# Kernel optimization log

Hardware: AMD Instinct MI355X
Metric: run time of the kernel (lower is better)

The kernel has to match this reference:

```python
import jax, jax.numpy as jnp
import numpy as np

INIT_L = 512.0
EPS = 1e-6
N_HEAD = 16


def fire_bias(T, w1, b1, w2, b2, c, L_multiplier):
    # positions and relative distances
    pos = jnp.arange(T, dtype=jnp.float32)
    rel = pos[:, None] - pos[None, :]                      # (T, T)
    threshold = jnp.abs(L_multiplier * INIT_L)
    pos_norm = jnp.maximum(pos, threshold)[:, None]        # (T, 1)
    rel = jnp.log(jnp.abs(c * rel) + 1.0)                  # (T, T)
    pos_norm = jnp.log(jnp.abs(c * pos_norm) + 1.0) + EPS  # (T, 1)
    nd = rel / pos_norm                                    # (T, T)
    # tiny MLP: 1 -> mlp_width -> n_head
    h = jax.nn.relu(nd[..., None] * w1[0] + b1)            # (T, T, 32)
    bias = jnp.einsum('tsw,wh->hts', h, w2) + b2[:, None, None]  # (H, T, T)
    causal = jnp.tril(jnp.ones((T, T), dtype=bool))
    bias = jnp.where(causal[None], bias, -jnp.inf)
    return bias[None]                                      # (1, H, T, T)


def reference(x, Wqkv, bqkv, Wproj, bproj, w1, b1, w2, b2, c_param, L_multiplier):
    B, T, C = x.shape
    H = N_HEAD
    hd = C // H
    qkv = x @ Wqkv + bqkv                                  # (B, T, 3C)
    q, k, v = jnp.split(qkv, 3, axis=-1)
    q = q.reshape(B, T, H, hd).transpose(0, 2, 1, 3)       # (B, H, T, hd)
    k = k.reshape(B, T, H, hd).transpose(0, 2, 1, 3)
    v = v.reshape(B, T, H, hd).transpose(0, 2, 1, 3)
    bias = fire_bias(T, w1, b1, w2, b2, c_param, L_multiplier)  # (1, H, T, T)
    scale = 1.0 / jnp.sqrt(jnp.float32(hd))
    att = jnp.einsum('bhqd,bhkd->bhqk', q, k) * scale + bias
    att = jax.nn.softmax(att, axis=-1)
    y = jnp.einsum('bhqk,bhkd->bhqd', att, v)              # (B, H, T, hd)
    y = y.transpose(0, 2, 1, 3).reshape(B, T, C)
    return y @ Wproj + bproj


def setup_inputs() -> dict:
    key = jax.random.key(0)
    ks = jax.random.split(key, 8)
    B, T, C, H, W = 2, 2048, 1024, 16, 32
    s = 0.02
    return {
        'x': jax.random.normal(ks[0], (B, T, C), jnp.float32),
        'Wqkv': jax.random.normal(ks[1], (C, 3 * C), jnp.float32) * s,
        'bqkv': jnp.zeros((3 * C,), jnp.float32),
        'Wproj': jax.random.normal(ks[2], (C, C), jnp.float32) * s,
        'bproj': jnp.zeros((C,), jnp.float32),
        'w1': jax.random.normal(ks[3], (1, W), jnp.float32),
        'b1': jnp.zeros((W,), jnp.float32),
        'w2': jax.random.normal(ks[4], (W, H), jnp.float32) * 0.1,
        'b2': jnp.zeros((H,), jnp.float32),
        'c_param': jnp.float32(0.1),
        'L_multiplier': jnp.float32(1.0),
    }
```

## Files before the change

kernel.cpp:

```cpp
#include <hip/hip_runtime.h>
#include <cstdint>

typedef unsigned short u16;
typedef unsigned int u32;

typedef short bf16x8 __attribute__((ext_vector_type(8)));
typedef float f32x4 __attribute__((ext_vector_type(4)));

#define LN2 0.69314718055994530942f
#define LOG2E 1.44269504088896340736f
#define INFF __builtin_inff()

__device__ __forceinline__ u16 f2bf(float f) {
  u32 u = __float_as_uint(f);
  u = (u + 0x7fffu + ((u >> 16) & 1u)) >> 16;
  return (u16)u;
}
__device__ __forceinline__ u32 pack2bf(float a, float b) {
  u32 ta = __float_as_uint(a) + 0x8000u;
  u32 tb = __float_as_uint(b) + 0x8000u;
  return __builtin_amdgcn_perm(tb, ta, 0x07060302u);
}
__device__ __forceinline__ u32 pack2bf_rne(float a, float b) {
  return (u32)f2bf(a) | ((u32)f2bf(b) << 16);
}

#if __has_builtin(__builtin_amdgcn_global_load_lds)
#define HAVE_GLDS 1
__device__ __forceinline__ void glds16(const u16* g, u16* l) {
  __builtin_amdgcn_global_load_lds((const __attribute__((address_space(1))) void*)g,
                                   (__attribute__((address_space(3))) void*)l, 16, 0, 0);
}
#else
#define HAVE_GLDS 0
#endif

__device__ __forceinline__ void stage1k(const u16* gperlane, u16* lwave, int lane) {
#if HAVE_GLDS
  (void)lane;
  glds16(gperlane, lwave);
#else
  *(uint4*)(lwave + lane * 8) = *(const uint4*)gperlane;
#endif
}

__device__ __forceinline__ u16* swzp(u16* base, int row, int bc) {
  return (u16*)((char*)base + row * 128 + (bc ^ ((row & 7) << 4)));
}


__global__ void k_convert_x(const float* __restrict__ in, u16* __restrict__ out, int n4) {
  int i = blockIdx.x * blockDim.x + threadIdx.x;
  if (i < n4) {
    float4 v = ((const float4*)in)[i];
    ushort4 o;
    o.x = f2bf(v.x); o.y = f2bf(v.y); o.z = f2bf(v.z); o.w = f2bf(v.w);
    ((ushort4*)out)[i] = o;
  }
}

__global__ void k_transpose_bf(const float* __restrict__ in, u16* __restrict__ out, int R, int C) {
  __shared__ float t[32][33];
  int c0 = blockIdx.x * 32, r0 = blockIdx.y * 32;
  int tx = threadIdx.x, ty = threadIdx.y;
#pragma unroll
  for (int k = 0; k < 4; k++) t[ty + 8 * k][tx] = in[(size_t)(r0 + ty + 8 * k) * C + c0 + tx];
  __syncthreads();
#pragma unroll
  for (int k = 0; k < 4; k++) out[(size_t)(c0 + ty + 8 * k) * R + r0 + tx] = f2bf(t[tx][ty + 8 * k]);
}

__global__ void k_tables(const float* __restrict__ cP, const float* __restrict__ lP,
                         float* __restrict__ ig2, float* __restrict__ rl) {
  int t = blockIdx.x * blockDim.x + threadIdx.x;
  float c = fabsf(cP[0]);
  if (t < 2048) {
    float lm = lP[0];
    float thr = fabsf(lm * 512.0f);
    float pn = fmaxf((float)t, thr);
    float den = logf(c * pn + 1.0f) + 1e-6f;
    ig2[t] = LN2 / den;
  }
  if (t < 2112) {
    int d = t - 63;
    if (d < 0) d = 0;
    rl[t] = log2f(c * (float)d + 1.0f);
  }
}

__global__ void k_segments(const float* __restrict__ w1, const float* __restrict__ b1,
                           const float* __restrict__ w2, const float* __restrict__ b2,
                           float* __restrict__ segX, float* __restrict__ segA,
                           float* __restrict__ segB, int* __restrict__ segU) {
  __shared__ float xs[32];
  __shared__ float srt[32];
  __shared__ float uniq[32];
  __shared__ int uCnt;
  int t = threadIdx.x;
  if (t < 32) {
    float w = w1[t], b = b1[t];
    xs[t] = (w != 0.0f) ? (-b / w) : INFF;
  }
  __syncthreads();
  if (t < 32) {
    float x = xs[t];
    int r = 0;
    for (int v = 0; v < 32; v++) {
      float xv = xs[v];
      if (xv < x || (xv == x && v < t)) r++;
    }
    srt[r] = x;
  }
  __syncthreads();
  if (t == 0) {
    int u = 0;
    for (int i = 0; i < 32; i++) {
      float v = srt[i];
      if (v < 3.0e38f && (u == 0 || v != uniq[u - 1])) uniq[u++] = v;
    }
    uCnt = u;
    segU[0] = u;
  }
  __syncthreads();
  int u = uCnt;
  if (t < u) segX[t] = uniq[t];
  for (int idx = t; idx < (u + 1) * 16; idx += blockDim.x) {
    int j = idx >> 4, h = idx & 15;
    float p;
    if (u == 0) p = 0.0f;
    else if (j == 0) p = uniq[0] - 1.0f;
    else if (j == u) p = uniq[u - 1] + 1.0f;
    else p = 0.5f * (uniq[j - 1] + uniq[j]);
    float A = b2[h], B = 0.0f;
    for (int w = 0; w < 32; w++) {
      float w1w = w1[w], b1w = b1[w], w2wh = w2[w * 16 + h];
      if (w1w != 0.0f) {
        if (fmaf(w1w, p, b1w) > 0.0f) { B += w1w * w2wh; A += b1w * w2wh; }
      } else if (b1w > 0.0f) {
        A += b1w * w2wh;
      }
    }
    segA[j * 16 + h] = A;
    segB[j * 16 + h] = B;
  }
}

template <int MODE, int BN>
__launch_bounds__(256, 3)
__global__ void k_gemm(const u16* __restrict__ A, const u16* __restrict__ BT,
                       const float* __restrict__ bias, float* __restrict__ outF,
                       u16* __restrict__ outQ, u16* __restrict__ outK, u16* __restrict__ outV,
                       int M, int N, int K) {
  constexpr int NT = BN / 32;
  constexpr int NCH = BN / 32;
  __shared__ u16 As[128 * 64];
  __shared__ u16 Bs[BN * 64];
  const int tid = threadIdx.x;
  const int lane = tid & 63, wave = tid >> 6;
  const int li = lane & 15, quad = lane >> 4;
  const int wrow = (wave >> 1) * 64, wcol = (wave & 1) * (BN / 2);
  const int rb = blockIdx.y * 128, cb = blockIdx.x * BN;

  f32x4 acc[4][NT];
#pragma unroll
  for (int i = 0; i < 4; i++)
#pragma unroll
    for (int j = 0; j < NT; j++) acc[i][j] = (f32x4){0.f, 0.f, 0.f, 0.f};

#if HAVE_GLDS
  const u16* gA = A + (size_t)(rb + (tid >> 3)) * K + (tid & 7) * 8;
  const u16* gB = BT + (size_t)(cb + (tid >> 3)) * K + (tid & 7) * 8;
  u16* lA = As + wave * 512;
  u16* lB = Bs + wave * 512;

  for (int k0 = 0; k0 < K; k0 += 64) {
    __syncthreads();
#pragma unroll
    for (int ch = 0; ch < 4; ch++) glds16(gA + (size_t)ch * 32 * K + k0, lA + ch * 2048);
#pragma unroll
    for (int ch = 0; ch < NCH; ch++) glds16(gB + (size_t)ch * 32 * K + k0, lB + ch * 2048);
    __syncthreads();
#pragma unroll
    for (int c = 0; c < 2; c++) {
      bf16x8 af[4], bfr[NT];
#pragma unroll
      for (int mt = 0; mt < 4; mt++)
        af[mt] = *(const bf16x8*)(&As[(wrow + mt * 16 + li) * 64 + c * 32 + quad * 8]);
#pragma unroll
      for (int nt = 0; nt < NT; nt++)
        bfr[nt] = *(const bf16x8*)(&Bs[(wcol + nt * 16 + li) * 64 + c * 32 + quad * 8]);
#pragma unroll
      for (int mt = 0; mt < 4; mt++)
#pragma unroll
        for (int nt = 0; nt < NT; nt++)
          acc[mt][nt] = __builtin_amdgcn_mfma_f32_16x16x32_bf16(af[mt], bfr[nt], acc[mt][nt], 0, 0, 0);
    }
  }
#else
  for (int k0 = 0; k0 < K; k0 += 64) {
    __syncthreads();
    for (int idx = tid * 8; idx < 128 * 64; idx += 256 * 8) {
      int rr = idx >> 6, cc = idx & 63;
      *(uint4*)(&As[idx]) = *(const uint4*)(A + (size_t)(rb + rr) * K + k0 + cc);
    }
    for (int idx = tid * 8; idx < BN * 64; idx += 256 * 8) {
      int rr = idx >> 6, cc = idx & 63;
      *(uint4*)(&Bs[idx]) = *(const uint4*)(BT + (size_t)(cb + rr) * K + k0 + cc);
    }
    __syncthreads();
#pragma unroll
    for (int c = 0; c < 2; c++) {
      bf16x8 af[4], bfr[NT];
#pragma unroll
      for (int mt = 0; mt < 4; mt++)
        af[mt] = *(const bf16x8*)(&As[(wrow + mt * 16 + li) * 64 + c * 32 + quad * 8]);
#pragma unroll
      for (int nt = 0; nt < NT; nt++)
        bfr[nt] = *(const bf16x8*)(&Bs[(wcol + nt * 16 + li) * 64 + c * 32 + quad * 8]);
#pragma unroll
      for (int mt = 0; mt < 4; mt++)
#pragma unroll
        for (int nt = 0; nt < NT; nt++)
          acc[mt][nt] = __builtin_amdgcn_mfma_f32_16x16x32_bf16(af[mt], bfr[nt], acc[mt][nt], 0, 0, 0);
    }
  }
#endif

#pragma unroll
  for (int mt = 0; mt < 4; mt++)
#pragma unroll
    for (int nt = 0; nt < NT; nt++) {
      const int col = cb + wcol + nt * 16 + li;
      const int row0 = rb + wrow + mt * 16 + quad * 4;
      float v[4];
#pragma unroll
      for (int r = 0; r < 4; r++) v[r] = acc[mt][nt][r] + bias[col];
      if (MODE == 0) {
        const int bb = row0 >> 11, tt0 = row0 & 2047;
        const int sel = col >> 10, w = col & 1023, hh = w >> 6, dd = w & 63;
        if (sel == 0) {
          u16* dst = outQ + ((size_t)((bb * 16 + hh) * 2048 + tt0)) * 64 + dd;
#pragma unroll
          for (int r = 0; r < 4; r++) dst[(size_t)r * 64] = f2bf(v[r]);
        } else if (sel == 1) {
          u16* base = outK + ((size_t)((bb * 16 + hh) * 2048 + tt0)) * 64;
#pragma unroll
          for (int r = 0; r < 4; r++) {
            int tt = tt0 + r;
            base[(size_t)r * 64 + (dd ^ (((tt & 7)) << 3))] = f2bf(v[r]);
          }
        } else {
          u16* vrow = outV + ((size_t)((bb * 16 + hh) * 64 + dd)) * 2048;
          uint2 pk;
          pk.x = pack2bf_rne(v[0], v[1]);
          pk.y = pack2bf_rne(v[2], v[3]);
          *(uint2*)(vrow + (tt0 ^ ((dd & 7) << 3))) = pk;
        }
      } else {
#pragma unroll
        for (int r = 0; r < 4; r++) outF[(size_t)(row0 + r) * N + col] = v[r];
      }
    }
}

__launch_bounds__(256, 3)
__global__ void k_attn(const u16* __restrict__ Q, const u16* __restrict__ K,
                       const u16* __restrict__ Vt, u16* __restrict__ Y,
                       const float* __restrict__ ig2, const float* __restrict__ RL,
                       const float* __restrict__ segX, const float* __restrict__ segA,
                       const float* __restrict__ segB, const int* __restrict__ segU) {
  __shared__ u16 KsB[2 * 64 * 64];
  __shared__ u16 VtsB[2 * 64 * 64];
  __shared__ u16 Ps[64 * 64];
  __shared__ float rls[2112];
  __shared__ float sXl[32];
  __shared__ float sAl[33];
  __shared__ float sBl[33];

  const int xi = blockIdx.x, h = blockIdx.y, b = blockIdx.z;
  const int q0b = xi >> 1;
  const int flip = (xi & 1) ^ ((h >> 3) & 1);
  const int qt = flip ? (31 - q0b) : q0b;

  const int tid = threadIdx.x, lane = tid & 63, wave = tid >> 6;
  const int li = lane & 15, quad = lane >> 4;
  const int bh = b * 16 + h;
  const u16* Qg = Q + (size_t)bh * 2048 * 64;
  const u16* Kg = K + (size_t)bh * 2048 * 64;
  const u16* Vg = Vt + (size_t)bh * 64 * 2048;

  for (int i = tid; i < 2112; i += 256) rls[i] = RL[i];

  const int u = segU[0];
  float x0 = INFF, A0, B0, A1, B1;
  A0 = segA[h]; B0 = segB[h]; A1 = A0; B1 = B0;
  if (u == 1) { x0 = segX[0]; A1 = segA[16 + h]; B1 = segB[16 + h]; }
  if (u > 1) {
    if (tid < u) sXl[tid] = segX[tid];
    if (tid < u + 1) { sAl[tid] = segA[tid * 16 + h]; sBl[tid] = segB[tid * 16 + h]; }
  }
  const float A0e = A0 * LOG2E, A1e = A1 * LOG2E;
  const float SCL = 0.125f * LOG2E;

  const int t = qt * 64 + wave * 16 + li;
  bf16x8 qf[2];
#pragma unroll
  for (int c = 0; c < 2; c++)
    qf[c] = *(const bf16x8*)(Qg + (size_t)t * 64 + c * 32 + quad * 8);

  const float gI = ig2[t];
  const float x0r = x0 / gI;
  const float B0g = B0 * gI * LOG2E, B1g = B1 * gI * LOG2E;
  const bool uniB = (u <= 1) && (x0r <= 0.0f) && (A0e == A1e);
  float mrow = -INFF, lrow = 0.0f;
  f32x4 oacc[4];
#pragma unroll
  for (int nt = 0; nt < 4; nt++) oacc[nt] = (f32x4){0.f, 0.f, 0.f, 0.f};

  const u16* kgB = Kg + (size_t)(wave * 16 + (lane >> 3)) * 64 + (lane & 7) * 8;
  const u16* vgB = Vg + (size_t)(wave * 16 + (lane >> 3)) * 2048 + (lane & 7) * 8;

  auto stage = [&](int buf, int kt2) {
    u16* kd = KsB + buf * 4096 + wave * 1024;
    const u16* kg = kgB + (size_t)kt2 * 4096;
    stage1k(kg, kd, lane);
    stage1k(kg + 8 * 64, kd + 512, lane);
    u16* vd = VtsB + buf * 4096 + wave * 1024;
    const u16* vg = vgB + kt2 * 64;
    stage1k(vg, vd, lane);
    stage1k(vg + 8 * 2048, vd + 512, lane);
  };

  stage(0, 0);
  int cur = 0;

  for (int kt = 0; kt <= qt; kt++) {
    const int kb = kt * 64;
    __syncthreads();
    if (kt < qt) stage(cur ^ 1, kt + 1);

    u16* KsT = KsB + cur * 4096;
    u16* VtT = VtsB + cur * 4096;

    f32x4 sacc[4];
#pragma unroll
    for (int nt = 0; nt < 4; nt++) sacc[nt] = (f32x4){0.f, 0.f, 0.f, 0.f};
#pragma unroll
    for (int c = 0; c < 2; c++)
#pragma unroll
      for (int nt = 0; nt < 4; nt++) {
        bf16x8 kf = *(const bf16x8*)swzp(KsT, nt * 16 + li, c * 64 + quad * 16);
        sacc[nt] = __builtin_amdgcn_mfma_f32_16x16x32_bf16(kf, qf[c], sacc[nt], 0, 0, 0);
      }

    const int Cbase = t - kb - quad * 4 + 63;
    const float* rp = &rls[Cbase - 51];
    const int lim = Cbase - 63;
    if (uniB) {
#pragma unroll
      for (int nt = 0; nt < 4; nt++)
#pragma unroll
        for (int r = 0; r < 4; r++) {
          float z = fmaf(rp[51 - nt * 16 - r], B1g, sacc[nt][r] * SCL);
          if (kt == qt) z = (nt * 16 + r > lim) ? -INFF : z;
          sacc[nt][r] = z;
        }
    } else if (u <= 1) {
#pragma unroll
      for (int nt = 0; nt < 4; nt++)
#pragma unroll
        for (int r = 0; r < 4; r++) {
          float rlv = rp[51 - nt * 16 - r];
          bool hi = rlv > x0r;
          float z = fmaf(rlv, hi ? B1g : B0g, hi ? A1e : A0e);
          z = fmaf(sacc[nt][r], SCL, z);
          if (kt == qt) z = (nt * 16 + r > lim) ? -INFF : z;
          sacc[nt][r] = z;
        }
    } else {
#pragma unroll
      for (int nt = 0; nt < 4; nt++)
#pragma unroll
        for (int r = 0; r < 4; r++) {
          float nd = rp[51 - nt * 16 - r] * gI;
          int j = 0;
          for (int i = 0; i < u; i++) j += (nd > sXl[i]) ? 1 : 0;
          float z = (fmaf(nd, sBl[j], sAl[j]) + sacc[nt][r] * 0.125f) * LOG2E;
          if (kt == qt) z = (nt * 16 + r > lim) ? -INFF : z;
          sacc[nt][r] = z;
        }
    }

    f32x4 mm = sacc[0];
#pragma unroll
    for (int nt = 1; nt < 4; nt++)
#pragma unroll
      for (int r = 0; r < 4; r++) mm[r] = fmaxf(mm[r], sacc[nt][r]);
    float vm = fmaxf(fmaxf(mm[0], mm[1]), fmaxf(mm[2], mm[3]));
    vm = fmaxf(vm, __shfl_xor(vm, 16, 64));
    vm = fmaxf(vm, __shfl_xor(vm, 32, 64));
    float mnew = fmaxf(mrow, vm);
    bool grew = mnew > mrow;
    float alpha = __builtin_amdgcn_exp2f(mrow - mnew);
    mrow = mnew;
#pragma unroll
    for (int nt = 0; nt < 4; nt++)
#pragma unroll
      for (int r = 0; r < 4; r++)
        sacc[nt][r] = __builtin_amdgcn_exp2f(sacc[nt][r] - mnew);
    f32x4 sv = (sacc[0] + sacc[1]) + (sacc[2] + sacc[3]);
    float s = (sv[0] + sv[1]) + (sv[2] + sv[3]);
    s += __shfl_xor(s, 16, 64);
    s += __shfl_xor(s, 32, 64);
    lrow = lrow * alpha + s;
    if (__any(grew)) {
#pragma unroll
      for (int nt = 0; nt < 4; nt++)
#pragma unroll
        for (int r = 0; r < 4; r++) oacc[nt][r] *= alpha;
    }

    const int prow = wave * 16 + li;
#pragma unroll
    for (int nt = 0; nt < 4; nt++) {
      uint2 pk;
      pk.x = pack2bf(sacc[nt][0], sacc[nt][1]);
      pk.y = pack2bf(sacc[nt][2], sacc[nt][3]);
      *(uint2*)swzp(Ps, prow, 32 * nt + 8 * quad) = pk;
    }

#pragma unroll
    for (int c = 0; c < 2; c++) {
      bf16x8 pf = *(const bf16x8*)swzp(Ps, prow, c * 64 + quad * 16);
#pragma unroll
      for (int nt = 0; nt < 4; nt++) {
        bf16x8 vf = *(const bf16x8*)swzp(VtT, nt * 16 + li, c * 64 + quad * 16);
        oacc[nt] = __builtin_amdgcn_mfma_f32_16x16x32_bf16(vf, pf, oacc[nt], 0, 0, 0);
      }
    }
    cur ^= 1;
  }

  float inv = 1.0f / lrow;
  u16* dst = Y + (size_t)(b * 2048 + t) * 1024 + h * 64 + quad * 4;
#pragma unroll
  for (int nt = 0; nt < 4; nt++) {
    uint2 pk;
    pk.x = pack2bf(oacc[nt][0] * inv, oacc[nt][1] * inv);
    pk.y = pack2bf(oacc[nt][2] * inv, oacc[nt][3] * inv);
    *(uint2*)(dst + nt * 16) = pk;
  }
}

extern "C" void kernel_launch(void* const* d_in, const int* in_sizes, int n_in,
                              void* d_out, int out_size, void* d_ws, size_t ws_size,
                              hipStream_t stream) {
  (void)in_sizes; (void)n_in; (void)out_size; (void)ws_size;
  const float* x = (const float*)d_in[0];
  const float* Wqkv = (const float*)d_in[1];
  const float* bqkv = (const float*)d_in[2];
  const float* Wproj = (const float*)d_in[3];
  const float* bproj = (const float*)d_in[4];
  const float* w1 = (const float*)d_in[5];
  const float* b1 = (const float*)d_in[6];
  const float* w2 = (const float*)d_in[7];
  const float* b2 = (const float*)d_in[8];
  const float* cP = (const float*)d_in[9];
  const float* lP = (const float*)d_in[10];

  char* ws = (char*)d_ws;
  u16* Xbf = (u16*)(ws);
  u16* WqkvT = (u16*)(ws + (size_t)(8 << 20));
  u16* WprojT = (u16*)(ws + (size_t)(14 << 20));
  u16* Qb = (u16*)(ws + (size_t)(16 << 20));
  u16* Kb = (u16*)(ws + (size_t)(24 << 20));
  u16* Vb = (u16*)(ws + (size_t)(32 << 20));
  u16* Yb = (u16*)(ws + (size_t)(40 << 20));
  float* IG = (float*)(ws + (size_t)(48 << 20));
  float* RL = IG + 2048;
  float* SEGX = RL + 2112;
  float* SEGA = SEGX + 32;
  float* SEGB = SEGA + 33 * 16;
  int* SEGU = (int*)(SEGB + 33 * 16);

  k_convert_x<<<4096, 256, 0, stream>>>(x, Xbf, 1048576);
  k_transpose_bf<<<dim3(96, 32), dim3(32, 8), 0, stream>>>(Wqkv, WqkvT, 1024, 3072);
  k_transpose_bf<<<dim3(32, 32), dim3(32, 8), 0, stream>>>(Wproj, WprojT, 1024, 1024);
  k_tables<<<9, 256, 0, stream>>>(cP, lP, IG, RL);
  k_segments<<<1, 64, 0, stream>>>(w1, b1, w2, b2, SEGX, SEGA, SEGB, SEGU);

  k_gemm<0, 128><<<dim3(24, 32), 256, 0, stream>>>(Xbf, WqkvT, bqkv, nullptr, Qb, Kb, Vb,
                                                   4096, 3072, 1024);
  k_attn<<<dim3(32, 16, 2), 256, 0, stream>>>(Qb, Kb, Vb, Yb, IG, RL, SEGX, SEGA, SEGB, SEGU);
  k_gemm<1, 64><<<dim3(16, 32), 256, 0, stream>>>(Yb, WprojT, bproj, (float*)d_out, nullptr,
                                                  nullptr, nullptr, 4096, 1024, 1024);
}
```

Measured before the change: 239.9 us.

## Process two query tiles per attention block and compute log distances inline

Result: slower. 247.3 us (+3.1%).

```diff
diff --git a/kernel.cpp b/kernel.cpp
--- a/kernel.cpp
+++ b/kernel.cpp
@@ -71,7 +71,7 @@
 }
 
 __global__ void k_tables(const float* __restrict__ cP, const float* __restrict__ lP,
-                         float* __restrict__ ig2, float* __restrict__ rl) {
+                         float* __restrict__ ig2) {
   int t = blockIdx.x * blockDim.x + threadIdx.x;
   float c = fabsf(cP[0]);
   if (t < 2048) {
@@ -80,11 +80,6 @@
     float pn = fmaxf((float)t, thr);
     float den = logf(c * pn + 1.0f) + 1e-6f;
     ig2[t] = LN2 / den;
-  }
-  if (t < 2112) {
-    int d = t - 63;
-    if (d < 0) d = 0;
-    rl[t] = log2f(c * (float)d + 1.0f);
   }
 }
 
@@ -263,24 +258,23 @@
     }
 }
 
-__launch_bounds__(256, 3)
+__launch_bounds__(256, 2)
 __global__ void k_attn(const u16* __restrict__ Q, const u16* __restrict__ K,
                        const u16* __restrict__ Vt, u16* __restrict__ Y,
-                       const float* __restrict__ ig2, const float* __restrict__ RL,
+                       const float* __restrict__ ig2, const float* __restrict__ cP,
                        const float* __restrict__ segX, const float* __restrict__ segA,
                        const float* __restrict__ segB, const int* __restrict__ segU) {
-  __shared__ u16 KsB[2 * 64 * 64];
-  __shared__ u16 VtsB[2 * 64 * 64];
-  __shared__ u16 Ps[64 * 64];
-  __shared__ float rls[2112];
+  __shared__ u16 KsB[2 * 4096];
+  __shared__ u16 VtsB[2 * 4096];
+  __shared__ u16 Ps[128 * 64];
   __shared__ float sXl[32];
   __shared__ float sAl[33];
   __shared__ float sBl[33];
 
   const int xi = blockIdx.x, h = blockIdx.y, b = blockIdx.z;
-  const int q0b = xi >> 1;
-  const int flip = (xi & 1) ^ ((h >> 3) & 1);
-  const int qt = flip ? (31 - q0b) : q0b;
+  const int flip = (b ^ (h >> 3)) & 1;
+  const int j = flip ? (15 - xi) : xi;
+  const int qt0 = 2 * j, qt1 = 2 * j + 1, ntiles = 2 * j + 2;
 
   const int tid = threadIdx.x, lane = tid & 63, wave = tid >> 6;
   const int li = lane & 15, quad = lane >> 4;
@@ -289,8 +283,7 @@
   const u16* Kg = K + (size_t)bh * 2048 * 64;
   const u16* Vg = Vt + (size_t)bh * 64 * 2048;
 
-  for (int i = tid; i < 2112; i += 256) rls[i] = RL[i];
-
+  const float cAbs = fabsf(cP[0]);
   const int u = segU[0];
   float x0 = INFF, A0, B0, A1, B1;
   A0 = segA[h]; B0 = segB[h]; A1 = A0; B1 = B0;
@@ -301,21 +294,28 @@
   }
   const float A0e = A0 * LOG2E, A1e = A1 * LOG2E;
   const float SCL = 0.125f * LOG2E;
-
-  const int t = qt * 64 + wave * 16 + li;
-  bf16x8 qf[2];
-#pragma unroll
-  for (int c = 0; c < 2; c++)
-    qf[c] = *(const bf16x8*)(Qg + (size_t)t * 64 + c * 32 + quad * 8);
-
-  const float gI = ig2[t];
-  const float x0r = x0 / gI;
-  const float B0g = B0 * gI * LOG2E, B1g = B1 * gI * LOG2E;
-  const bool uniB = (u <= 1) && (x0r <= 0.0f) && (A0e == A1e);
-  float mrow = -INFF, lrow = 0.0f;
-  f32x4 oacc[4];
-#pragma unroll
-  for (int nt = 0; nt < 4; nt++) oacc[nt] = (f32x4){0.f, 0.f, 0.f, 0.f};
+  const bool uniB = (u <= 1) && (x0 <= 0.0f) && (A0e == A1e);
+
+  const int t0 = j * 128 + wave * 16 + li;
+  const int t1 = t0 + 64;
+  bf16x8 qf0[2], qf1[2];
+#pragma unroll
+  for (int c = 0; c < 2; c++) {
+    qf0[c] = *(const bf16x8*)(Qg + (size_t)t0 * 64 + c * 32 + quad * 8);
+    qf1[c] = *(const bf16x8*)(Qg + (size_t)t1 * 64 + c * 32 + quad * 8);
+  }
+  const float gI0 = ig2[t0], gI1 = ig2[t1];
+  const float x0r0 = x0 / gI0, x0r1 = x0 / gI1;
+  const float B0g0 = B0 * gI0 * LOG2E, B1g0 = B1 * gI0 * LOG2E;
+  const float B0g1 = B0 * gI1 * LOG2E, B1g1 = B1 * gI1 * LOG2E;
+
+  float m0 = -INFF, l0 = 0.0f, m1 = -INFF, l1 = 0.0f;
+  f32x4 o0[4], o1[4];
+#pragma unroll
+  for (int nt = 0; nt < 4; nt++) {
+    o0[nt] = (f32x4){0.f, 0.f, 0.f, 0.f};
+    o1[nt] = (f32x4){0.f, 0.f, 0.f, 0.f};
+  }
 
   const u16* kgB = Kg + (size_t)(wave * 16 + (lane >> 3)) * 64 + (lane & 7) * 8;
   const u16* vgB = Vg + (size_t)(wave * 16 + (lane >> 3)) * 2048 + (lane & 7) * 8;
@@ -334,121 +334,182 @@
   stage(0, 0);
   int cur = 0;
 
-  for (int kt = 0; kt <= qt; kt++) {
+  for (int kt = 0; kt < ntiles; kt++) {
     const int kb = kt * 64;
     __syncthreads();
-    if (kt < qt) stage(cur ^ 1, kt + 1);
+    if (kt + 1 < ntiles) stage(cur ^ 1, kt + 1);
 
     u16* KsT = KsB + cur * 4096;
     u16* VtT = VtsB + cur * 4096;
 
-    f32x4 sacc[4];
-#pragma unroll
-    for (int nt = 0; nt < 4; nt++) sacc[nt] = (f32x4){0.f, 0.f, 0.f, 0.f};
+    f32x4 s0[4], s1[4];
+#pragma unroll
+    for (int nt = 0; nt < 4; nt++) {
+      s0[nt] = (f32x4){0.f, 0.f, 0.f, 0.f};
+      s1[nt] = (f32x4){0.f, 0.f, 0.f, 0.f};
+    }
+    __builtin_amdgcn_s_setprio(1);
 #pragma unroll
     for (int c = 0; c < 2; c++)
 #pragma unroll
       for (int nt = 0; nt < 4; nt++) {
         bf16x8 kf = *(const bf16x8*)swzp(KsT, nt * 16 + li, c * 64 + quad * 16);
-        sacc[nt] = __builtin_amdgcn_mfma_f32_16x16x32_bf16(kf, qf[c], sacc[nt], 0, 0, 0);
+        s0[nt] = __builtin_amdgcn_mfma_f32_16x16x32_bf16(kf, qf0[c], s0[nt], 0, 0, 0);
+        s1[nt] = __builtin_amdgcn_mfma_f32_16x16x32_bf16(kf, qf1[c], s1[nt], 0, 0, 0);
       }
-
-    const int Cbase = t - kb - quad * 4 + 63;
-    const float* rp = &rls[Cbase - 51];
-    const int lim = Cbase - 63;
+    __builtin_amdgcn_s_setprio(0);
+
+    const float dq0 = (float)(t0 - kb - quad * 4);
+    const float dq1 = dq0 + 64.0f;
     if (uniB) {
 #pragma unroll
       for (int nt = 0; nt < 4; nt++)
 #pragma unroll
         for (int r = 0; r < 4; r++) {
-          float z = fmaf(rp[51 - nt * 16 - r], B1g, sacc[nt][r] * SCL);
-          if (kt == qt) z = (nt * 16 + r > lim) ? -INFF : z;
-          sacc[nt][r] = z;
+          float rl0 = __builtin_amdgcn_logf(fmaf(cAbs, dq0 - nt * 16 - r, 1.0f));
+          float rl1 = __builtin_amdgcn_logf(fmaf(cAbs, dq1 - nt * 16 - r, 1.0f));
+          s0[nt][r] = fmaf(rl0, B1g0, s0[nt][r] * SCL);
+          s1[nt][r] = fmaf(rl1, B1g1, s1[nt][r] * SCL);
         }
     } else if (u <= 1) {
 #pragma unroll
       for (int nt = 0; nt < 4; nt++)
 #pragma unroll
         for (int r = 0; r < 4; r++) {
-          float rlv = rp[51 - nt * 16 - r];
-          bool hi = rlv > x0r;
-          float z = fmaf(rlv, hi ? B1g : B0g, hi ? A1e : A0e);
-          z = fmaf(sacc[nt][r], SCL, z);
-          if (kt == qt) z = (nt * 16 + r > lim) ? -INFF : z;
-          sacc[nt][r] = z;
+          float rl0 = __builtin_amdgcn_logf(fmaf(cAbs, dq0 - nt * 16 - r, 1.0f));
+          float rl1 = __builtin_amdgcn_logf(fmaf(cAbs, dq1 - nt * 16 - r, 1.0f));
+          bool h0 = rl0 > x0r0, h1 = rl1 > x0r1;
+          float z0 = fmaf(rl0, h0 ? B1g0 : B0g0, h0 ? A1e : A0e);
+          float z1 = fmaf(rl1, h1 ? B1g1 : B0g1, h1 ? A1e : A0e);
+          s0[nt][r] = fmaf(s0[nt][r], SCL, z0);
+          s1[nt][r] = fmaf(s1[nt][r], SCL, z1);
         }
     } else {
 #pragma unroll
       for (int nt = 0; nt < 4; nt++)
 #pragma unroll
         for (int r = 0; r < 4; r++) {
-          float nd = rp[51 - nt * 16 - r] * gI;
-          int j = 0;
-          for (int i = 0; i < u; i++) j += (nd > sXl[i]) ? 1 : 0;
-          float z = (fmaf(nd, sBl[j], sAl[j]) + sacc[nt][r] * 0.125f) * LOG2E;
-          if (kt == qt) z = (nt * 16 + r > lim) ? -INFF : z;
-          sacc[nt][r] = z;
+          float rl0 = __builtin_amdgcn_logf(fmaf(cAbs, dq0 - nt * 16 - r, 1.0f));
+          float rl1 = __builtin_amdgcn_logf(fmaf(cAbs, dq1 - nt * 16 - r, 1.0f));
+          float nd0 = rl0 * gI0, nd1 = rl1 * gI1;
+          int j0 = 0, j1 = 0;
+          for (int i = 0; i < u; i++) {
+            j0 += (nd0 > sXl[i]) ? 1 : 0;
+            j1 += (nd1 > sXl[i]) ? 1 : 0;
+          }
+          s0[nt][r] = (fmaf(nd0, sBl[j0], sAl[j0]) + s0[nt][r] * 0.125f) * LOG2E;
+          s1[nt][r] = (fmaf(nd1, sBl[j1], sAl[j1]) + s1[nt][r] * 0.125f) * LOG2E;
         }
     }
 
-    f32x4 mm = sacc[0];
-#pragma unroll
-    for (int nt = 1; nt < 4; nt++)
-#pragma unroll
-      for (int r = 0; r < 4; r++) mm[r] = fmaxf(mm[r], sacc[nt][r]);
-    float vm = fmaxf(fmaxf(mm[0], mm[1]), fmaxf(mm[2], mm[3]));
-    vm = fmaxf(vm, __shfl_xor(vm, 16, 64));
-    vm = fmaxf(vm, __shfl_xor(vm, 32, 64));
-    float mnew = fmaxf(mrow, vm);
-    bool grew = mnew > mrow;
-    float alpha = __builtin_amdgcn_exp2f(mrow - mnew);
-    mrow = mnew;
-#pragma unroll
-    for (int nt = 0; nt < 4; nt++)
-#pragma unroll
-      for (int r = 0; r < 4; r++)
-        sacc[nt][r] = __builtin_amdgcn_exp2f(sacc[nt][r] - mnew);
-    f32x4 sv = (sacc[0] + sacc[1]) + (sacc[2] + sacc[3]);
-    float s = (sv[0] + sv[1]) + (sv[2] + sv[3]);
-    s += __shfl_xor(s, 16, 64);
-    s += __shfl_xor(s, 32, 64);
-    lrow = lrow * alpha + s;
-    if (__any(grew)) {
+    if (kt >= qt0) {
+      const int lim0 = t0 - kb - quad * 4;
 #pragma unroll
       for (int nt = 0; nt < 4; nt++)
 #pragma unroll
-        for (int r = 0; r < 4; r++) oacc[nt][r] *= alpha;
-    }
-
-    const int prow = wave * 16 + li;
+        for (int r = 0; r < 4; r++)
+          if (nt * 16 + r > lim0) s0[nt][r] = -INFF;
+    }
+    if (kt == qt1) {
+      const int lim1 = t1 - kb - quad * 4;
+#pragma unroll
+      for (int nt = 0; nt < 4; nt++)
+#pragma unroll
+        for (int r = 0; r < 4; r++)
+          if (nt * 16 + r > lim1) s1[nt][r] = -INFF;
+    }
+
+    {
+      f32x4 mm0 = s0[0], mm1 = s1[0];
+#pragma unroll
+      for (int nt = 1; nt < 4; nt++)
+#pragma unroll
+        for (int r = 0; r < 4; r++) {
+          mm0[r] = fmaxf(mm0[r], s0[nt][r]);
+          mm1[r] = fmaxf(mm1[r], s1[nt][r]);
+        }
+      float v0 = fmaxf(fmaxf(mm0[0], mm0[1]), fmaxf(mm0[2], mm0[3]));
+      float v1 = fmaxf(fmaxf(mm1[0], mm1[1]), fmaxf(mm1[2], mm1[3]));
+      v0 = fmaxf(v0, __shfl_xor(v0, 16, 64));
+      v1 = fmaxf(v1, __shfl_xor(v1, 16, 64));
+      v0 = fmaxf(v0, __shfl_xor(v0, 32, 64));
+      v1 = fmaxf(v1, __shfl_xor(v1, 32, 64));
+      float mn0 = fmaxf(m0, v0), mn1 = fmaxf(m1, v1);
+      bool g0 = mn0 > m0, g1 = mn1 > m1;
+      float a0 = __builtin_amdgcn_exp2f(m0 - mn0);
+      float a1 = __builtin_amdgcn_exp2f(m1 - mn1);
+      m0 = mn0; m1 = mn1;
+#pragma unroll
+      for (int nt = 0; nt < 4; nt++)
+#pragma unroll
+        for (int r = 0; r < 4; r++) {
+          s0[nt][r] = __builtin_amdgcn_exp2f(s0[nt][r] - mn0);
+          s1[nt][r] = __builtin_amdgcn_exp2f(s1[nt][r] - mn1);
+        }
+      f32x4 sv0 = (s0[0] + s0[1]) + (s0[2] + s0[3]);
+      f32x4 sv1 = (s1[0] + s1[1]) + (s1[2] + s1[3]);
+      float ss0 = (sv0[0] + sv0[1]) + (sv0[2] + sv0[3]);
+      float ss1 = (sv1[0] + sv1[1]) + (sv1[2] + sv1[3]);
+      ss0 += __shfl_xor(ss0, 16, 64);
+      ss1 += __shfl_xor(ss1, 16, 64);
+      ss0 += __shfl_xor(ss0, 32, 64);
+      ss1 += __shfl_xor(ss1, 32, 64);
+      l0 = l0 * a0 + ss0;
+      l1 = l1 * a1 + ss1;
+      if (__any(g0)) {
+#pragma unroll
+        for (int nt = 0; nt < 4; nt++)
+#pragma unroll
+          for (int r = 0; r < 4; r++) o0[nt][r] *= a0;
+      }
+      if (__any(g1)) {
+#pragma unroll
+        for (int nt = 0; nt < 4; nt++)
+#pragma unroll
+          for (int r = 0; r < 4; r++) o1[nt][r] *= a1;
+      }
+    }
+
+    const int pr0 = wave * 16 + li, pr1 = pr0 + 64;
 #pragma unroll
     for (int nt = 0; nt < 4; nt++) {
-      uint2 pk;
-      pk.x = pack2bf(sacc[nt][0], sacc[nt][1]);
-      pk.y = pack2bf(sacc[nt][2], sacc[nt][3]);
-      *(uint2*)swzp(Ps, prow, 32 * nt + 8 * quad) = pk;
-    }
-
+      uint2 pk0, pk1;
+      pk0.x = pack2bf(s0[nt][0], s0[nt][1]);
+      pk0.y = pack2bf(s0[nt][2], s0[nt][3]);
+      pk1.x = pack2bf(s1[nt][0], s1[nt][1]);
+      pk1.y = pack2bf(s1[nt][2], s1[nt][3]);
+      *(uint2*)swzp(Ps, pr0, 32 * nt + 8 * quad) = pk0;
+      *(uint2*)swzp(Ps, pr1, 32 * nt + 8 * quad) = pk1;
+    }
+
+    __builtin_amdgcn_s_setprio(1);
 #pragma unroll
     for (int c = 0; c < 2; c++) {
-      bf16x8 pf = *(const bf16x8*)swzp(Ps, prow, c * 64 + quad * 16);
+      bf16x8 pf0 = *(const bf16x8*)swzp(Ps, pr0, c * 64 + quad * 16);
+      bf16x8 pf1 = *(const bf16x8*)swzp(Ps, pr1, c * 64 + quad * 16);
 #pragma unroll
       for (int nt = 0; nt < 4; nt++) {
         bf16x8 vf = *(const bf16x8*)swzp(VtT, nt * 16 + li, c * 64 + quad * 16);
-        oacc[nt] = __builtin_amdgcn_mfma_f32_16x16x32_bf16(vf, pf, oacc[nt], 0, 0, 0);
+        o0[nt] = __builtin_amdgcn_mfma_f32_16x16x32_bf16(vf, pf0, o0[nt], 0, 0, 0);
+        o1[nt] = __builtin_amdgcn_mfma_f32_16x16x32_bf16(vf, pf1, o1[nt], 0, 0, 0);
       }
     }
+    __builtin_amdgcn_s_setprio(0);
     cur ^= 1;
   }
 
-  float inv = 1.0f / lrow;
-  u16* dst = Y + (size_t)(b * 2048 + t) * 1024 + h * 64 + quad * 4;
+  const float i0 = 1.0f / l0, i1 = 1.0f / l1;
+  u16* d0 = Y + (size_t)(b * 2048 + t0) * 1024 + h * 64 + quad * 4;
+  u16* d1 = Y + (size_t)(b * 2048 + t1) * 1024 + h * 64 + quad * 4;
 #pragma unroll
   for (int nt = 0; nt < 4; nt++) {
-    uint2 pk;
-    pk.x = pack2bf(oacc[nt][0] * inv, oacc[nt][1] * inv);
-    pk.y = pack2bf(oacc[nt][2] * inv, oacc[nt][3] * inv);
-    *(uint2*)(dst + nt * 16) = pk;
+    uint2 pk0, pk1;
+    pk0.x = pack2bf(o0[nt][0] * i0, o0[nt][1] * i0);
+    pk0.y = pack2bf(o0[nt][2] * i0, o0[nt][3] * i0);
+    pk1.x = pack2bf(o1[nt][0] * i1, o1[nt][1] * i1);
+    pk1.y = pack2bf(o1[nt][2] * i1, o1[nt][3] * i1);
+    *(uint2*)(d0 + nt * 16) = pk0;
+    *(uint2*)(d1 + nt * 16) = pk1;
   }
 }
 
@@ -477,8 +538,7 @@
   u16* Vb = (u16*)(ws + (size_t)(32 << 20));
   u16* Yb = (u16*)(ws + (size_t)(40 << 20));
   float* IG = (float*)(ws + (size_t)(48 << 20));
-  float* RL = IG + 2048;
-  float* SEGX = RL + 2112;
+  float* SEGX = IG + 2048;
   float* SEGA = SEGX + 32;
   float* SEGB = SEGA + 33 * 16;
   int* SEGU = (int*)(SEGB + 33 * 16);
@@ -486,12 +546,12 @@
   k_convert_x<<<4096, 256, 0, stream>>>(x, Xbf, 1048576);
   k_transpose_bf<<<dim3(96, 32), dim3(32, 8), 0, stream>>>(Wqkv, WqkvT, 1024, 3072);
   k_transpose_bf<<<dim3(32, 32), dim3(32, 8), 0, stream>>>(Wproj, WprojT, 1024, 1024);
-  k_tables<<<9, 256, 0, stream>>>(cP, lP, IG, RL);
+  k_tables<<<8, 256, 0, stream>>>(cP, lP, IG);
   k_segments<<<1, 64, 0, stream>>>(w1, b1, w2, b2, SEGX, SEGA, SEGB, SEGU);
 
   k_gemm<0, 128><<<dim3(24, 32), 256, 0, stream>>>(Xbf, WqkvT, bqkv, nullptr, Qb, Kb, Vb,
                                                    4096, 3072, 1024);
-  k_attn<<<dim3(32, 16, 2), 256, 0, stream>>>(Qb, Kb, Vb, Yb, IG, RL, SEGX, SEGA, SEGB, SEGU);
+  k_attn<<<dim3(16, 16, 2), 256, 0, stream>>>(Qb, Kb, Vb, Yb, IG, cP, SEGX, SEGA, SEGB, SEGU);
   k_gemm<1, 64><<<dim3(16, 32), 256, 0, stream>>>(Yb, WprojT, bproj, (float*)d_out, nullptr,
                                                   nullptr, nullptr, 4096, 1024, 1024);
 }
```
